# Optimization experiments

Hardware: AMD Instinct MI355X
Metric: run time of the kernel (lower is better)

Reference implementation:

```python
import jax, jax.numpy as jnp
import numpy as np

N = 100000      # nodes
E = 1600000     # edges (avg degree 16)
IN = 256        # input feature dim
F1 = 32         # hidden per-head dim
H = 4           # heads layer 1
C = 40          # num classes (layer 2, 1 head)
NEG_SLOPE = 0.2 # DGL GATConv default


def setup_inputs() -> dict:
    key = jax.random.key(0)
    ks = jax.random.split(key, 12)
    feat = jax.random.normal(ks[0], (N, IN), jnp.float32)
    src = jax.random.randint(ks[1], (E,), 0, N, dtype=jnp.int32)
    dst = jax.random.randint(ks[2], (E,), 0, N, dtype=jnp.int32)
    # Xavier-ish scaled params
    W1 = jax.random.normal(ks[3], (IN, H * F1), jnp.float32) / np.sqrt(IN)
    al1 = jax.random.normal(ks[4], (H, F1), jnp.float32) / np.sqrt(F1)
    ar1 = jax.random.normal(ks[5], (H, F1), jnp.float32) / np.sqrt(F1)
    b1 = jnp.zeros((H * F1,), jnp.float32)
    W2 = jax.random.normal(ks[6], (H * F1, C), jnp.float32) / np.sqrt(H * F1)
    al2 = jax.random.normal(ks[7], (1, C), jnp.float32) / np.sqrt(C)
    ar2 = jax.random.normal(ks[8], (1, C), jnp.float32) / np.sqrt(C)
    b2 = jnp.zeros((C,), jnp.float32)
    return {"features": feat, "src": src, "dst": dst,
            "W1": W1, "al1": al1, "ar1": ar1, "b1": b1,
            "W2": W2, "al2": al2, "ar2": ar2, "b2": b2}


def gat_layer(x, src, dst, W, al, ar, b, heads, fdim):
    # Linear projection, split into heads: (N, H, F)
    h = (x @ W).reshape(-1, heads, fdim)
    # Per-node attention halves: (N, H)
    el = jnp.sum(h * al, axis=-1)
    er = jnp.sum(h * ar, axis=-1)
    # Edge scores: LeakyReLU(el[src] + er[dst]) -> (E, H)
    e = jax.nn.leaky_relu(el[src] + er[dst], negative_slope=NEG_SLOPE)
    # Edge softmax over incoming edges of each dst node
    m = jax.ops.segment_max(e, dst, num_segments=N)           # (N, H)
    ee = jnp.exp(e - m[dst])                                  # (E, H)
    ssum = jax.ops.segment_sum(ee, dst, num_segments=N)       # (N, H)
    alpha = ee / ssum[dst]                                    # (E, H)
    # Weighted scatter-add aggregation: (N, H, F)
    out = jax.ops.segment_sum(alpha[:, :, None] * h[src], dst, num_segments=N)
    return out + b.reshape(heads, fdim)


def reference(features, src, dst, W1, al1, ar1, b1, W2, al2, ar2, b2):
    x = gat_layer(features, src, dst, W1, al1, ar1, b1, H, F1)
    x = jax.nn.elu(x.reshape(-1, H * F1))                     # (N, H*F1)
    out = gat_layer(x, src, dst, W2, al2, ar2, b2, 1, C)      # (N, 1, C)
    return out.mean(axis=1)                                   # (N, C)
```

## Files before the change

### kernel.cpp

```cpp
#include <hip/hip_runtime.h>
#include <math.h>

typedef unsigned int u32;
typedef __attribute__((ext_vector_type(8))) short bf16x8;
typedef __attribute__((ext_vector_type(4))) float floatx4;

constexpr int NN = 100000;
constexpr int EE = 1600000;
constexpr int IND = 256;
constexpr int F1 = 32;
constexpr int HF = 128;
constexpr int C  = 40;
constexpr float SLOPE = 0.2f;

constexpr int CAP = 64;
constexpr int H2ROW = 32;

constexpr int G1_BLOCKS  = (NN + 127) / 128;
constexpr int HB_BLOCKS  = (EE / 4 + 255) / 256;
constexpr int FAT_BLOCKS = G1_BLOCKS + HB_BLOCKS;

__device__ __forceinline__ float bf_lo(u32 v) { return __uint_as_float(v << 16); }
__device__ __forceinline__ float bf_hi(u32 v) { return __uint_as_float(v & 0xffff0000u); }

__device__ __forceinline__ u32 pkbf(float lo, float hi) {
    u32 r;
    asm("v_cvt_pk_bf16_f32 %0, %1, %2" : "=v"(r) : "v"(lo), "v"(hi));
    return r;
}

__global__ __launch_bounds__(256) void k_g1h(const float* __restrict__ feat,
                                             const float* __restrict__ W1,
                                             const float* __restrict__ al1,
                                             const float* __restrict__ ar1,
                                             u32* __restrict__ h1b,
                                             float* __restrict__ el1,
                                             float* __restrict__ er1,
                                             const int* __restrict__ dst,
                                             int* __restrict__ cnt,
                                             int* __restrict__ rank) {
    __shared__ u32 w1t[128 * 128];
    const int bx = blockIdx.x;
    const int tid = threadIdx.x;

    if (bx % 3 != 0) {
        const int hb = bx - bx / 3 - 1;
        const int e = (hb * 256 + tid) * 4;
        if (e < EE) {
            const int4 d4 = *(const int4*)&dst[e];
            int4 r4;
            r4.x = atomicAdd(&cnt[d4.x], 1);
            r4.y = atomicAdd(&cnt[d4.y], 1);
            r4.z = atomicAdd(&cnt[d4.z], 1);
            r4.w = atomicAdd(&cnt[d4.w], 1);
            *(int4*)&rank[e] = r4;
        }
        return;
    }

    const int bid = bx / 3;
    {
        const int n = tid & 127;
        const int o0 = (tid >> 7) * 16;
        for (int i = 0; i < 16; ++i) {
            const int o = o0 + i;
            float f0 = W1[(size_t)(o * 8 + 0) * HF + n];
            float f1 = W1[(size_t)(o * 8 + 1) * HF + n];
            float f2 = W1[(size_t)(o * 8 + 2) * HF + n];
            float f3 = W1[(size_t)(o * 8 + 3) * HF + n];
            float f4 = W1[(size_t)(o * 8 + 4) * HF + n];
            float f5 = W1[(size_t)(o * 8 + 5) * HF + n];
            float f6 = W1[(size_t)(o * 8 + 6) * HF + n];
            float f7 = W1[(size_t)(o * 8 + 7) * HF + n];
            uint4 p;
            p.x = pkbf(f0, f1);
            p.y = pkbf(f2, f3);
            p.z = pkbf(f4, f5);
            p.w = pkbf(f6, f7);
            *(uint4*)&w1t[n * 128 + ((o ^ (n & 7)) << 2)] = p;
        }
    }
    __syncthreads();

    const int w = tid >> 6, lane = tid & 63;
    const int quad = lane >> 4, l15 = lane & 15;
    const int rbase = bid * 128 + w * 32;

    float alv[4][2], arv[4][2];
    #pragma unroll
    for (int h = 0; h < 4; ++h) {
        alv[h][0] = al1[h * F1 + l15];
        alv[h][1] = al1[h * F1 + 16 + l15];
        arv[h][0] = ar1[h * F1 + l15];
        arv[h][1] = ar1[h * F1 + 16 + l15];
    }

    floatx4 acc[2][8] = {};
    for (int ks = 0; ks < 8; ++ks) {
        bf16x8 a[2];
        #pragma unroll
        for (int ri = 0; ri < 2; ++ri) {
            int row = rbase + ri * 16 + l15;
            row = row < NN ? row : NN - 1;
            const size_t base = (size_t)row * IND + ks * 32 + quad * 8;
            const float4 f0 = *(const float4*)&feat[base];
            const float4 f1 = *(const float4*)&feat[base + 4];
            uint4 p;
            p.x = pkbf(f0.x, f0.y);
            p.y = pkbf(f0.z, f0.w);
            p.z = pkbf(f1.x, f1.y);
            p.w = pkbf(f1.z, f1.w);
            a[ri] = *(bf16x8*)&p;
        }
        const int g = ks * 4 + quad;
        #pragma unroll
        for (int ci = 0; ci < 8; ++ci) {
            const int n = ci * 16 + l15;
            uint4 bw = *(const uint4*)&w1t[n * 128 + ((g ^ (n & 7)) << 2)];
            bf16x8 b = *(bf16x8*)&bw;
            acc[0][ci] = __builtin_amdgcn_mfma_f32_16x16x32_bf16(a[0], b, acc[0][ci], 0, 0, 0);
            acc[1][ci] = __builtin_amdgcn_mfma_f32_16x16x32_bf16(a[1], b, acc[1][ci], 0, 0, 0);
        }
    }

    #pragma unroll
    for (int ri = 0; ri < 2; ++ri) {
        #pragma unroll
        for (int r = 0; r < 4; ++r) {
            const int row = rbase + ri * 16 + quad * 4 + r;
            const bool rok = row < NN;
            #pragma unroll
            for (int h = 0; h < 4; ++h) {
                float pe = acc[ri][2 * h][r] * alv[h][0] + acc[ri][2 * h + 1][r] * alv[h][1];
                float pr = acc[ri][2 * h][r] * arv[h][0] + acc[ri][2 * h + 1][r] * arv[h][1];
                #pragma unroll
                for (int m = 1; m < 16; m <<= 1) {
                    pe += __shfl_xor(pe, m, 64);
                    pr += __shfl_xor(pr, m, 64);
                }
                if (l15 == 0 && rok) {
                    el1[row * 4 + h] = pe;
                    er1[row * 4 + h] = pr;
                }
            }
            #pragma unroll
            for (int ci = 0; ci < 8; ++ci) {
                float v = acc[ri][ci][r];
                float vn = __shfl_xor(v, 1, 64);
                if (!(lane & 1) && rok) {
                    h1b[(size_t)row * 64 + ci * 8 + (l15 >> 1)] = pkbf(v, vn);
                }
            }
        }
    }
}

__global__ __launch_bounds__(256) void k_bscat(const int* __restrict__ src,
                                               const int* __restrict__ dst,
                                               const int* __restrict__ rank,
                                               int* __restrict__ colp) {
    const int e = (blockIdx.x * 256 + threadIdx.x) * 4;
    if (e < EE) {
        const int4 d4 = *(const int4*)&dst[e];
        const int4 s4 = *(const int4*)&src[e];
        const int4 r4 = *(const int4*)&rank[e];
        colp[(d4.x << 6) + r4.x] = s4.x;
        colp[(d4.y << 6) + r4.y] = s4.y;
        colp[(d4.z << 6) + r4.z] = s4.z;
        colp[(d4.w << 6) + r4.w] = s4.w;
    }
}

__global__ __launch_bounds__(256) void k_agg1(const int* __restrict__ cnt,
                                              const int* __restrict__ colp,
                                              const u32* __restrict__ h1b,
                                              const float* __restrict__ el1,
                                              const float* __restrict__ er1,
                                              const float* __restrict__ b1,
                                              u32* __restrict__ x_b) {
    const int lane = threadIdx.x & 63, wid = threadIdx.x >> 6;
    const int g = lane >> 4, li = lane & 15;
    const int d = blockIdx.x * 16 + wid * 4 + g;
    const int head = li >> 2;
    const float erd = er1[d * 4 + head];
    const int beg = d << 6;
    const int end = beg + cnt[d];
    const u32 li16 = (u32)li << 4;
    const u32 hoff = (u32)head << 2;

    float a0 = 0.f, a1 = 0.f, a2 = 0.f, a3 = 0.f;
    float a4 = 0.f, a5 = 0.f, a6 = 0.f, a7 = 0.f;
    float ssum = 0.f;

    auto body = [&](int e) {
        const bool act = e < end;
        int s = colp[act ? e : beg];
        s = act ? s : 0;
        const u32 rb = (u32)s << 8;
        const uint4 v = *(const uint4*)((const char*)h1b + (rb + li16));
        float c = *(const float*)((const char*)el1 + (((u32)s << 4) + hoff)) + erd;
        c = fmaxf(c, SLOPE * c);
        float w = __expf(c);
        w = act ? w : 0.f;
        ssum += w;
        a0 += w * bf_lo(v.x); a1 += w * bf_hi(v.x);
        a2 += w * bf_lo(v.y); a3 += w * bf_hi(v.y);
        a4 += w * bf_lo(v.z); a5 += w * bf_hi(v.z);
        a6 += w * bf_lo(v.w); a7 += w * bf_hi(v.w);
    };

    int e = beg;
    while (__any(e < end)) {
        body(e);
        body(e + 1);
        body(e + 2);
        body(e + 3);
        e += 4;
    }

    const float inv = ssum > 0.f ? 1.f / ssum : 0.f;
    const float4 ba = *(const float4*)&b1[8 * li];
    const float4 bb = *(const float4*)&b1[8 * li + 4];
    float r0 = a0 * inv + ba.x, r1 = a1 * inv + ba.y;
    float r2 = a2 * inv + ba.z, r3 = a3 * inv + ba.w;
    float r4 = a4 * inv + bb.x, r5 = a5 * inv + bb.y;
    float r6 = a6 * inv + bb.z, r7 = a7 * inv + bb.w;
    r0 = r0 > 0.f ? r0 : __expf(r0) - 1.f;
    r1 = r1 > 0.f ? r1 : __expf(r1) - 1.f;
    r2 = r2 > 0.f ? r2 : __expf(r2) - 1.f;
    r3 = r3 > 0.f ? r3 : __expf(r3) - 1.f;
    r4 = r4 > 0.f ? r4 : __expf(r4) - 1.f;
    r5 = r5 > 0.f ? r5 : __expf(r5) - 1.f;
    r6 = r6 > 0.f ? r6 : __expf(r6) - 1.f;
    r7 = r7 > 0.f ? r7 : __expf(r7) - 1.f;
    uint4 p;
    p.x = pkbf(r0, r1);
    p.y = pkbf(r2, r3);
    p.z = pkbf(r4, r5);
    p.w = pkbf(r6, r7);
    *(uint4*)&x_b[(size_t)d * 64 + 4 * li] = p;
}

__global__ __launch_bounds__(256) void k_gemm2(const u32* __restrict__ x_b,
                                               const float* __restrict__ W2,
                                               const float* __restrict__ al2,
                                               const float* __restrict__ ar2,
                                               u32* __restrict__ h2b,
                                               float* __restrict__ er2) {
    __shared__ u32 w2t[48 * 64];
    const int tid = threadIdx.x;
    {
        const int o = tid & 15;
        const int n0 = tid >> 4;
        for (int n = n0; n < 48; n += 16) {
            float f[8];
            #pragma unroll
            for (int j = 0; j < 8; ++j) {
                const int k = o * 8 + j;
                float v;
                if (n < C) v = W2[(size_t)k * C + n];
                else if (n == 40) {
                    v = 0.f;
                    for (int c = 0; c < C; ++c) v += W2[(size_t)k * C + c] * al2[c];
                } else if (n == 41) {
                    v = 0.f;
                    for (int c = 0; c < C; ++c) v += W2[(size_t)k * C + c] * ar2[c];
                } else v = 0.f;
                f[j] = v;
            }
            uint4 p;
            p.x = pkbf(f[0], f[1]);
            p.y = pkbf(f[2], f[3]);
            p.z = pkbf(f[4], f[5]);
            p.w = pkbf(f[6], f[7]);
            *(uint4*)&w2t[n * 64 + ((o ^ (n & 7)) << 2)] = p;
        }
    }
    __syncthreads();

    const int w = tid >> 6, lane = tid & 63;
    const int quad = lane >> 4, l15 = lane & 15;
    const int rbase = blockIdx.x * 128 + w * 32;
    floatx4 acc[2][3] = {};

    #pragma unroll
    for (int ks = 0; ks < 4; ++ks) {
        bf16x8 a[2];
        #pragma unroll
        for (int ri = 0; ri < 2; ++ri) {
            int row = rbase + ri * 16 + l15;
            row = row < NN ? row : NN - 1;
            uint4 ax = *(const uint4*)&x_b[(size_t)row * 64 + ks * 16 + quad * 4];
            a[ri] = *(bf16x8*)&ax;
        }
        const int g = ks * 4 + quad;
        #pragma unroll
        for (int ci = 0; ci < 3; ++ci) {
            const int n = ci * 16 + l15;
            uint4 bw = *(const uint4*)&w2t[n * 64 + ((g ^ (n & 7)) << 2)];
            bf16x8 b = *(bf16x8*)&bw;
            acc[0][ci] = __builtin_amdgcn_mfma_f32_16x16x32_bf16(a[0], b, acc[0][ci], 0, 0, 0);
            acc[1][ci] = __builtin_amdgcn_mfma_f32_16x16x32_bf16(a[1], b, acc[1][ci], 0, 0, 0);
        }
    }

    #pragma unroll
    for (int ri = 0; ri < 2; ++ri) {
        #pragma unroll
        for (int r = 0; r < 4; ++r) {
            const int row = rbase + ri * 16 + quad * 4 + r;
            const bool rok = row < NN;
            #pragma unroll
            for (int ci = 0; ci < 3; ++ci) {
                float v = acc[ri][ci][r];
                float vn = __shfl_xor(v, 1, 64);
                if (rok) {
                    if (ci < 2) {
                        if (!(lane & 1))
                            h2b[(size_t)row * H2ROW + ci * 8 + (l15 >> 1)] = pkbf(v, vn);
                    } else {
                        if (!(lane & 1) && l15 < 8)
                            h2b[(size_t)row * H2ROW + 16 + (l15 >> 1)] = pkbf(v, vn);
                        else if (l15 == 8)
                            h2b[(size_t)row * H2ROW + 20] = __float_as_uint(v);
                        else if (l15 == 9)
                            er2[row] = v;
                    }
                }
            }
        }
    }
}

__global__ __launch_bounds__(256) void k_agg2(const int* __restrict__ cnt,
                                              const int* __restrict__ colp,
                                              const u32* __restrict__ h2b,
                                              const float* __restrict__ er2,
                                              const float* __restrict__ b2,
                                              float* __restrict__ out) {
    const int lane = threadIdx.x & 63, wid = threadIdx.x >> 6;
    const int g = lane >> 4, li = lane & 15;
    const int d = blockIdx.x * 16 + wid * 4 + g;
    const float erd = er2[d];
    const int beg = d << 6;
    const int end = beg + cnt[d];
    const u32 ob = (u32)(li < 12 ? 2 * li : 22) << 2;

    float a0 = 0.f, a1 = 0.f, a2 = 0.f, a3 = 0.f;
    float ssum = 0.f;

    auto body = [&](int e) {
        const bool act = e < end;
        int s = colp[act ? e : beg];
        s = act ? s : 0;
        const u32 rb = (u32)s << 7;
        const uint2 v = *(const uint2*)((const char*)h2b + (rb + ob));
        float c = *(const float*)((const char*)h2b + rb + 80) + erd;
        c = fmaxf(c, SLOPE * c);
        float w = __expf(c);
        w = act ? w : 0.f;
        ssum += w;
        a0 += w * bf_lo(v.x); a1 += w * bf_hi(v.x);
        a2 += w * bf_lo(v.y); a3 += w * bf_hi(v.y);
    };

    int e = beg;
    while (__any(e < end)) {
        body(e);
        body(e + 1);
        body(e + 2);
        body(e + 3);
        e += 4;
    }

    if (li < 10) {
        const float inv = ssum > 0.f ? 1.f / ssum : 0.f;
        const float4 b = *(const float4*)&b2[4 * li];
        float4 r;
        r.x = a0 * inv + b.x;
        r.y = a1 * inv + b.y;
        r.z = a2 * inv + b.z;
        r.w = a3 * inv + b.w;
        *(float4*)&out[(size_t)d * C + 4 * li] = r;
    }
}

extern "C" void kernel_launch(void* const* d_in, const int* in_sizes, int n_in,
                              void* d_out, int out_size, void* d_ws, size_t ws_size,
                              hipStream_t stream) {
    const float* feat = (const float*)d_in[0];
    const int*   src  = (const int*)d_in[1];
    const int*   dst  = (const int*)d_in[2];
    const float* W1   = (const float*)d_in[3];
    const float* al1  = (const float*)d_in[4];
    const float* ar1  = (const float*)d_in[5];
    const float* b1   = (const float*)d_in[6];
    const float* W2   = (const float*)d_in[7];
    const float* al2  = (const float*)d_in[8];
    const float* ar2  = (const float*)d_in[9];
    const float* b2   = (const float*)d_in[10];
    float* out = (float*)d_out;

    u32*   h1b = (u32*)d_ws;
    u32*   x_b = h1b + (size_t)NN * 64;
    float* el1 = (float*)(x_b + (size_t)NN * 64);
    float* er1 = el1 + (size_t)NN * 4;
    int* cnt   = (int*)(er1 + (size_t)NN * 4);
    int* colp  = cnt + NN;
    int* rank  = (int*)x_b;
    u32*   h2b = h1b;
    float* er2 = er1;

    hipMemsetAsync(cnt, 0, (size_t)NN * sizeof(int), stream);
    k_g1h<<<FAT_BLOCKS, 256, 0, stream>>>(feat, W1, al1, ar1, h1b, el1, er1,
                                          dst, cnt, rank);
    k_bscat<<<(EE / 4 + 255) / 256, 256, 0, stream>>>(src, dst, rank, colp);

    k_agg1<<<NN / 16, 256, 0, stream>>>(cnt, colp, h1b, el1, er1, b1, x_b);

    k_gemm2<<<(NN + 127) / 128, 256, 0, stream>>>(x_b, W2, al2, ar2, h2b, er2);
    k_agg2<<<NN / 16, 256, 0, stream>>>(cnt, colp, h2b, er2, b2, out);
}
```

Baseline: 381.9 us.

## Fuse layer-2 projection GEMM into layer-1 aggregation and halve W1 LDS staging

```diff
diff --git a/kernel.cpp b/kernel.cpp
--- a/kernel.cpp
+++ b/kernel.cpp
@@ -39,7 +39,7 @@
                                              const int* __restrict__ dst,
                                              int* __restrict__ cnt,
                                              int* __restrict__ rank) {
-    __shared__ u32 w1t[128 * 128];
+    __shared__ u32 w1t[128 * 64];
     const int bx = blockIdx.x;
     const int tid = threadIdx.x;
 
@@ -59,29 +59,6 @@
     }
 
     const int bid = bx / 3;
-    {
-        const int n = tid & 127;
-        const int o0 = (tid >> 7) * 16;
-        for (int i = 0; i < 16; ++i) {
-            const int o = o0 + i;
-            float f0 = W1[(size_t)(o * 8 + 0) * HF + n];
-            float f1 = W1[(size_t)(o * 8 + 1) * HF + n];
-            float f2 = W1[(size_t)(o * 8 + 2) * HF + n];
-            float f3 = W1[(size_t)(o * 8 + 3) * HF + n];
-            float f4 = W1[(size_t)(o * 8 + 4) * HF + n];
-            float f5 = W1[(size_t)(o * 8 + 5) * HF + n];
-            float f6 = W1[(size_t)(o * 8 + 6) * HF + n];
-            float f7 = W1[(size_t)(o * 8 + 7) * HF + n];
-            uint4 p;
-            p.x = pkbf(f0, f1);
-            p.y = pkbf(f2, f3);
-            p.z = pkbf(f4, f5);
-            p.w = pkbf(f6, f7);
-            *(uint4*)&w1t[n * 128 + ((o ^ (n & 7)) << 2)] = p;
-        }
-    }
-    __syncthreads();
-
     const int w = tid >> 6, lane = tid & 63;
     const int quad = lane >> 4, l15 = lane & 15;
     const int rbase = bid * 128 + w * 32;
@@ -96,31 +73,58 @@
     }
 
     floatx4 acc[2][8] = {};
-    for (int ks = 0; ks < 8; ++ks) {
-        bf16x8 a[2];
-        #pragma unroll
-        for (int ri = 0; ri < 2; ++ri) {
-            int row = rbase + ri * 16 + l15;
-            row = row < NN ? row : NN - 1;
-            const size_t base = (size_t)row * IND + ks * 32 + quad * 8;
-            const float4 f0 = *(const float4*)&feat[base];
-            const float4 f1 = *(const float4*)&feat[base + 4];
-            uint4 p;
-            p.x = pkbf(f0.x, f0.y);
-            p.y = pkbf(f0.z, f0.w);
-            p.z = pkbf(f1.x, f1.y);
-            p.w = pkbf(f1.z, f1.w);
-            a[ri] = *(bf16x8*)&p;
-        }
-        const int g = ks * 4 + quad;
-        #pragma unroll
-        for (int ci = 0; ci < 8; ++ci) {
-            const int n = ci * 16 + l15;
-            uint4 bw = *(const uint4*)&w1t[n * 128 + ((g ^ (n & 7)) << 2)];
-            bf16x8 b = *(bf16x8*)&bw;
-            acc[0][ci] = __builtin_amdgcn_mfma_f32_16x16x32_bf16(a[0], b, acc[0][ci], 0, 0, 0);
-            acc[1][ci] = __builtin_amdgcn_mfma_f32_16x16x32_bf16(a[1], b, acc[1][ci], 0, 0, 0);
-        }
+    for (int pass = 0; pass < 2; ++pass) {
+        {
+            const int n = tid & 127;
+            const int o0 = (tid >> 7) * 8;
+            for (int i = 0; i < 8; ++i) {
+                const int o = o0 + i;
+                const int ko = pass * 16 + o;
+                float f0 = W1[(size_t)(ko * 8 + 0) * HF + n];
+                float f1 = W1[(size_t)(ko * 8 + 1) * HF + n];
+                float f2 = W1[(size_t)(ko * 8 + 2) * HF + n];
+                float f3 = W1[(size_t)(ko * 8 + 3) * HF + n];
+                float f4 = W1[(size_t)(ko * 8 + 4) * HF + n];
+                float f5 = W1[(size_t)(ko * 8 + 5) * HF + n];
+                float f6 = W1[(size_t)(ko * 8 + 6) * HF + n];
+                float f7 = W1[(size_t)(ko * 8 + 7) * HF + n];
+                uint4 p;
+                p.x = pkbf(f0, f1);
+                p.y = pkbf(f2, f3);
+                p.z = pkbf(f4, f5);
+                p.w = pkbf(f6, f7);
+                *(uint4*)&w1t[n * 64 + ((o ^ (n & 7)) << 2)] = p;
+            }
+        }
+        __syncthreads();
+        for (int ks = 0; ks < 4; ++ks) {
+            const int gk = pass * 4 + ks;
+            bf16x8 a[2];
+            #pragma unroll
+            for (int ri = 0; ri < 2; ++ri) {
+                int row = rbase + ri * 16 + l15;
+                row = row < NN ? row : NN - 1;
+                const size_t base = (size_t)row * IND + gk * 32 + quad * 8;
+                const float4 f0 = *(const float4*)&feat[base];
+                const float4 f1 = *(const float4*)&feat[base + 4];
+                uint4 p;
+                p.x = pkbf(f0.x, f0.y);
+                p.y = pkbf(f0.z, f0.w);
+                p.z = pkbf(f1.x, f1.y);
+                p.w = pkbf(f1.z, f1.w);
+                a[ri] = *(bf16x8*)&p;
+            }
+            const int g = ks * 4 + quad;
+            #pragma unroll
+            for (int ci = 0; ci < 8; ++ci) {
+                const int n = ci * 16 + l15;
+                uint4 bw = *(const uint4*)&w1t[n * 64 + ((g ^ (n & 7)) << 2)];
+                bf16x8 b = *(bf16x8*)&bw;
+                acc[0][ci] = __builtin_amdgcn_mfma_f32_16x16x32_bf16(a[0], b, acc[0][ci], 0, 0, 0);
+                acc[1][ci] = __builtin_amdgcn_mfma_f32_16x16x32_bf16(a[1], b, acc[1][ci], 0, 0, 0);
+            }
+        }
+        __syncthreads();
     }
 
     #pragma unroll
@@ -158,8 +162,41 @@
 __global__ __launch_bounds__(256) void k_bscat(const int* __restrict__ src,
                                                const int* __restrict__ dst,
                                                const int* __restrict__ rank,
-                                               int* __restrict__ colp) {
-    const int e = (blockIdx.x * 256 + threadIdx.x) * 4;
+                                               int* __restrict__ colp,
+                                               const float* __restrict__ W2,
+                                               const float* __restrict__ al2,
+                                               const float* __restrict__ ar2,
+                                               u32* __restrict__ w2g) {
+    const int tid = threadIdx.x;
+    if (blockIdx.x == HB_BLOCKS) {
+        const int o = tid & 15;
+        const int n0 = tid >> 4;
+        for (int n = n0; n < 48; n += 16) {
+            float f[8];
+            #pragma unroll
+            for (int j = 0; j < 8; ++j) {
+                const int k = o * 8 + j;
+                float v;
+                if (n < C) v = W2[(size_t)k * C + n];
+                else if (n == 40) {
+                    v = 0.f;
+                    for (int c = 0; c < C; ++c) v += W2[(size_t)k * C + c] * al2[c];
+                } else if (n == 41) {
+                    v = 0.f;
+                    for (int c = 0; c < C; ++c) v += W2[(size_t)k * C + c] * ar2[c];
+                } else v = 0.f;
+                f[j] = v;
+            }
+            uint4 p;
+            p.x = pkbf(f[0], f[1]);
+            p.y = pkbf(f[2], f[3]);
+            p.z = pkbf(f[4], f[5]);
+            p.w = pkbf(f[6], f[7]);
+            *(uint4*)&w2g[n * 64 + ((o ^ (n & 7)) << 2)] = p;
+        }
+        return;
+    }
+    const int e = (blockIdx.x * 256 + tid) * 4;
     if (e < EE) {
         const int4 d4 = *(const int4*)&dst[e];
         const int4 s4 = *(const int4*)&src[e];
@@ -171,13 +208,16 @@
     }
 }
 
-__global__ __launch_bounds__(256) void k_agg1(const int* __restrict__ cnt,
-                                              const int* __restrict__ colp,
-                                              const u32* __restrict__ h1b,
-                                              const float* __restrict__ el1,
-                                              const float* __restrict__ er1,
-                                              const float* __restrict__ b1,
-                                              u32* __restrict__ x_b) {
+__global__ __launch_bounds__(256) void k_agg1f(const int* __restrict__ cnt,
+                                               const int* __restrict__ colp,
+                                               const u32* __restrict__ h1b,
+                                               const float* __restrict__ el1,
+                                               const float* __restrict__ er1,
+                                               const float* __restrict__ b1,
+                                               const u32* __restrict__ w2g,
+                                               u32* __restrict__ h2b,
+                                               float* __restrict__ er2) {
+    __shared__ u32 xt[16][68];
     const int lane = threadIdx.x & 63, wid = threadIdx.x >> 6;
     const int g = lane >> 4, li = lane & 15;
     const int d = blockIdx.x * 16 + wid * 4 + g;
@@ -238,95 +278,38 @@
     p.y = pkbf(r2, r3);
     p.z = pkbf(r4, r5);
     p.w = pkbf(r6, r7);
-    *(uint4*)&x_b[(size_t)d * 64 + 4 * li] = p;
-}
-
-__global__ __launch_bounds__(256) void k_gemm2(const u32* __restrict__ x_b,
-                                               const float* __restrict__ W2,
-                                               const float* __restrict__ al2,
-                                               const float* __restrict__ ar2,
-                                               u32* __restrict__ h2b,
-                                               float* __restrict__ er2) {
-    __shared__ u32 w2t[48 * 64];
-    const int tid = threadIdx.x;
-    {
-        const int o = tid & 15;
-        const int n0 = tid >> 4;
-        for (int n = n0; n < 48; n += 16) {
-            float f[8];
-            #pragma unroll
-            for (int j = 0; j < 8; ++j) {
-                const int k = o * 8 + j;
-                float v;
-                if (n < C) v = W2[(size_t)k * C + n];
-                else if (n == 40) {
-                    v = 0.f;
-                    for (int c = 0; c < C; ++c) v += W2[(size_t)k * C + c] * al2[c];
-                } else if (n == 41) {
-                    v = 0.f;
-                    for (int c = 0; c < C; ++c) v += W2[(size_t)k * C + c] * ar2[c];
-                } else v = 0.f;
-                f[j] = v;
-            }
-            uint4 p;
-            p.x = pkbf(f[0], f[1]);
-            p.y = pkbf(f[2], f[3]);
-            p.z = pkbf(f[4], f[5]);
-            p.w = pkbf(f[6], f[7]);
-            *(uint4*)&w2t[n * 64 + ((o ^ (n & 7)) << 2)] = p;
-        }
-    }
+    *(uint4*)&xt[wid * 4 + g][4 * li] = p;
     __syncthreads();
 
-    const int w = tid >> 6, lane = tid & 63;
-    const int quad = lane >> 4, l15 = lane & 15;
-    const int rbase = blockIdx.x * 128 + w * 32;
-    floatx4 acc[2][3] = {};
-
-    #pragma unroll
-    for (int ks = 0; ks < 4; ++ks) {
-        bf16x8 a[2];
+    if (wid < 3) {
+        const int ci = wid;
+        const int quad = g;
+        const int n = ci * 16 + li;
+        floatx4 acc = {};
         #pragma unroll
-        for (int ri = 0; ri < 2; ++ri) {
-            int row = rbase + ri * 16 + l15;
-            row = row < NN ? row : NN - 1;
-            uint4 ax = *(const uint4*)&x_b[(size_t)row * 64 + ks * 16 + quad * 4];
-            a[ri] = *(bf16x8*)&ax;
-        }
-        const int g = ks * 4 + quad;
-        #pragma unroll
-        for (int ci = 0; ci < 3; ++ci) {
-            const int n = ci * 16 + l15;
-            uint4 bw = *(const uint4*)&w2t[n * 64 + ((g ^ (n & 7)) << 2)];
-            bf16x8 b = *(bf16x8*)&bw;
-            acc[0][ci] = __builtin_amdgcn_mfma_f32_16x16x32_bf16(a[0], b, acc[0][ci], 0, 0, 0);
-            acc[1][ci] = __builtin_amdgcn_mfma_f32_16x16x32_bf16(a[1], b, acc[1][ci], 0, 0, 0);
-        }
-    }
-
-    #pragma unroll
-    for (int ri = 0; ri < 2; ++ri) {
+        for (int ks = 0; ks < 4; ++ks) {
+            const uint4 ax = *(const uint4*)&xt[li][ks * 16 + quad * 4];
+            const bf16x8 a = *(const bf16x8*)&ax;
+            const int gg = ks * 4 + quad;
+            const uint4 bw = *(const uint4*)&w2g[n * 64 + ((gg ^ (n & 7)) << 2)];
+            const bf16x8 b = *(const bf16x8*)&bw;
+            acc = __builtin_amdgcn_mfma_f32_16x16x32_bf16(a, b, acc, 0, 0, 0);
+        }
         #pragma unroll
         for (int r = 0; r < 4; ++r) {
-            const int row = rbase + ri * 16 + quad * 4 + r;
-            const bool rok = row < NN;
-            #pragma unroll
-            for (int ci = 0; ci < 3; ++ci) {
-                float v = acc[ri][ci][r];
-                float vn = __shfl_xor(v, 1, 64);
-                if (rok) {
-                    if (ci < 2) {
-                        if (!(lane & 1))
-                            h2b[(size_t)row * H2ROW + ci * 8 + (l15 >> 1)] = pkbf(v, vn);
-                    } else {
-                        if (!(lane & 1) && l15 < 8)
-                            h2b[(size_t)row * H2ROW + 16 + (l15 >> 1)] = pkbf(v, vn);
-                        else if (l15 == 8)
-                            h2b[(size_t)row * H2ROW + 20] = __float_as_uint(v);
-                        else if (l15 == 9)
-                            er2[row] = v;
-                    }
-                }
+            const int row = blockIdx.x * 16 + quad * 4 + r;
+            const float v = acc[r];
+            const float vn = __shfl_xor(v, 1, 64);
+            if (ci < 2) {
+                if (!(lane & 1))
+                    h2b[(size_t)row * H2ROW + ci * 8 + (li >> 1)] = pkbf(v, vn);
+            } else {
+                if (!(lane & 1) && li < 8)
+                    h2b[(size_t)row * H2ROW + 16 + (li >> 1)] = pkbf(v, vn);
+                else if (li == 8)
+                    h2b[(size_t)row * H2ROW + 20] = __float_as_uint(v);
+                else if (li == 9)
+                    er2[row] = v;
             }
         }
     }
@@ -402,22 +385,24 @@
     float* out = (float*)d_out;
 
     u32*   h1b = (u32*)d_ws;
-    u32*   x_b = h1b + (size_t)NN * 64;
-    float* el1 = (float*)(x_b + (size_t)NN * 64);
+    u32*   xb2 = h1b + (size_t)NN * 64;
+    float* el1 = (float*)(xb2 + (size_t)NN * 64);
     float* er1 = el1 + (size_t)NN * 4;
     int* cnt   = (int*)(er1 + (size_t)NN * 4);
     int* colp  = cnt + NN;
-    int* rank  = (int*)x_b;
-    u32*   h2b = h1b;
-    float* er2 = er1;
+    float* er2 = (float*)(colp + (size_t)NN * CAP);
+    u32*   w2g = (u32*)(er2 + NN);
+    int* rank  = (int*)xb2;
+    u32*   h2b = xb2;
 
     hipMemsetAsync(cnt, 0, (size_t)NN * sizeof(int), stream);
     k_g1h<<<FAT_BLOCKS, 256, 0, stream>>>(feat, W1, al1, ar1, h1b, el1, er1,
                                           dst, cnt, rank);
-    k_bscat<<<(EE / 4 + 255) / 256, 256, 0, stream>>>(src, dst, rank, colp);
-
-    k_agg1<<<NN / 16, 256, 0, stream>>>(cnt, colp, h1b, el1, er1, b1, x_b);
-
-    k_gemm2<<<(NN + 127) / 128, 256, 0, stream>>>(x_b, W2, al2, ar2, h2b, er2);
+    k_bscat<<<HB_BLOCKS + 1, 256, 0, stream>>>(src, dst, rank, colp,
+                                               W2, al2, ar2, w2g);
+
+    k_agg1f<<<NN / 16, 256, 0, stream>>>(cnt, colp, h1b, el1, er1, b1,
+                                         w2g, h2b, er2);
+
     k_agg2<<<NN / 16, 256, 0, stream>>>(cnt, colp, h2b, er2, b2, out);
 }
```

Result: faster. 368.2 us (-3.6%).
